# Performance work log

Hardware: AMD Instinct MI355X
Metric: run time of the kernel (lower is better)

## Reference

```python
import jax, jax.numpy as jnp
import numpy as np

D = 1024
S = 2048
B = 4


def setup_inputs() -> dict:
    key = jax.random.key(0)
    ks = jax.random.split(key, 9)
    sc = 1.0 / np.sqrt(D)
    return {
        "x": jax.random.normal(ks[0], (B, S, D), dtype=jnp.float32),
        "Wq": jax.random.normal(ks[1], (D, D), dtype=jnp.float32) * sc,
        "bq": jax.random.normal(ks[2], (D,), dtype=jnp.float32) * 0.02,
        "Wk": jax.random.normal(ks[3], (D, D), dtype=jnp.float32) * sc,
        "bk": jax.random.normal(ks[4], (D,), dtype=jnp.float32) * 0.02,
        "Wv": jax.random.normal(ks[5], (D, D), dtype=jnp.float32) * sc,
        "bv": jax.random.normal(ks[6], (D,), dtype=jnp.float32) * 0.02,
        "Wp": jax.random.normal(ks[7], (D, D), dtype=jnp.float32) * sc,
        "bp": jax.random.normal(ks[8], (D,), dtype=jnp.float32) * 0.02,
    }


def reference(x, Wq, bq, Wk, bk, Wv, bv, Wp, bp):
    # torch nn.Linear: y = x @ W.T + b  (W stored [out, in])
    q = jnp.einsum("bsd,ed->bse", x, Wq) + bq  # [B,S,D]
    k = jnp.einsum("bsd,ed->bse", x, Wk) + bk
    v = jnp.einsum("bsd,ed->bse", x, Wv) + bv

    scale = 1.0 / jnp.sqrt(jnp.asarray(q.shape[-1], q.dtype))
    # single-head attention: contract over full embd_dim (no head split in source)
    scores = jnp.einsum("bqd,bkd->bqk", q, k) * scale  # [B,S,S]

    seq = x.shape[1]
    causal = jnp.tril(jnp.ones((seq, seq), dtype=bool))  # [S,S]
    scores = jnp.where(causal[None, :, :], scores, -jnp.inf)

    attn = jax.nn.softmax(scores, axis=-1)  # [B,S,S]
    out = jnp.einsum("bqk,bkd->bqd", attn, v)  # [B,S,D]
    out = jnp.einsum("bsd,ed->bse", out, Wp) + bp
    return out
```

## Files before the change

### kernel.cpp

```cpp
#include <hip/hip_runtime.h>

#define AS1(p) ((const __attribute__((address_space(1))) void*)(p))
#define AS3(p) ((__attribute__((address_space(3))) void*)(p))

typedef unsigned short u16;
typedef __bf16 bf16x8 __attribute__((ext_vector_type(8)));
typedef short s16x8 __attribute__((ext_vector_type(8)));
typedef float f32x4 __attribute__((ext_vector_type(4)));
typedef unsigned short u16x4 __attribute__((ext_vector_type(4)));

__device__ __forceinline__ u16 f2bf(float x) {
    unsigned u = __float_as_uint(x);
    unsigned r = (u + 0x7FFFu + ((u >> 16) & 1u)) >> 16;
    return (u16)r;
}

template <typename V8>
__device__ __forceinline__ auto mfma_sel(V8 a, V8 b, f32x4 c, int)
    -> decltype(__builtin_amdgcn_mfma_f32_16x16x32_bf16(a, b, c, 0, 0, 0))
{
    return __builtin_amdgcn_mfma_f32_16x16x32_bf16(a, b, c, 0, 0, 0);
}
template <typename V8>
__device__ __forceinline__ f32x4 mfma_sel(V8 a, V8 b, f32x4 c, long)
{
    s16x8 a2 = __builtin_bit_cast(s16x8, a);
    s16x8 b2 = __builtin_bit_cast(s16x8, b);
    return __builtin_amdgcn_mfma_f32_16x16x32_bf16(a2, b2, c, 0, 0, 0);
}
__device__ __forceinline__ f32x4 mfma16x16x32(bf16x8 a, bf16x8 b, f32x4 c)
{
    return mfma_sel(a, b, c, 0);
}

__global__ __launch_bounds__(256) void cvt_bf16_kernel(const float* __restrict__ in,
                                                       u16* __restrict__ out, int n4)
{
    int i = blockIdx.x * 256 + threadIdx.x;
    if (i >= n4) return;
    float4 f = ((const float4*)in)[i];
    u16x4 o;
    o.x = f2bf(f.x); o.y = f2bf(f.y); o.z = f2bf(f.z); o.w = f2bf(f.w);
    ((u16x4*)out)[i] = o;
}

__global__ __launch_bounds__(256) void cvt_w4_kernel(const float* __restrict__ Wq,
                                                     const float* __restrict__ Wk,
                                                     const float* __restrict__ Wv,
                                                     const float* __restrict__ Wp,
                                                     u16* __restrict__ Wcat,
                                                     u16* __restrict__ Wpb, int n4)
{
    int i = blockIdx.x * 256 + threadIdx.x;
    if (i >= n4) return;
    const int by = blockIdx.y;
    const float* src = (by == 0) ? Wq : (by == 1) ? Wk : (by == 2) ? Wv : Wp;
    u16* dst = (by == 3) ? Wpb : (Wcat + (size_t)by * n4 * 4);
    float4 f = ((const float4*)src)[i];
    u16x4 o;
    o.x = f2bf(f.x); o.y = f2bf(f.y); o.z = f2bf(f.z); o.w = f2bf(f.w);
    ((u16x4*)dst)[i] = o;
}

#define GBM 128
#define GBN 256
#define GBK 64
#define ABUF 16384
#define BBUF 32768
#define TBUF (ABUF + BBUF)
#define LDS_NT2 (3 * TBUF)

template <int BIAS, int OUTBF16, int CSKIP, int CKB>
__global__ __launch_bounds__(512, 2)
void gemm_nt2(const u16* __restrict__ A, const u16* __restrict__ B,
              void* __restrict__ Cv, const float* __restrict__ bias,
              void* __restrict__ C2, const float* __restrict__ bias2,
              void* __restrict__ C3, const float* __restrict__ bias3,
              int M, int N, int K, int lda, int ldb, int ldc,
              long long sA, long long sB, long long sC, float scale)
{
    extern __shared__ char smem[];

    int by = blockIdx.y;
    if (CKB) by = gridDim.y - 1 - by;
    const int m0 = by * GBM;
    const int n0 = blockIdx.x * GBN;
    if (CSKIP && n0 > m0 + GBM - 1) return;

    const int z = blockIdx.z;
    A += (size_t)z * (size_t)sA;
    B += (size_t)z * (size_t)sB;

    const int t = threadIdx.x;
    const int lane = t & 63;
    const int w = t >> 6;
    const int wr = w >> 2;
    const int wc = w & 3;
    const int fr = lane & 15, fg = lane >> 4;

    int Keff = K;
    if (CKB) { Keff = m0 + GBM; if (Keff > K) Keff = K; }
    const int nk = Keff / GBK;

    f32x4 acc[4][4] = {};

    auto STAGE = [&](int kt, int buf) {
        const int k0 = kt * GBK;
        char* sb = smem + buf * TBUF;
        #pragma unroll
        for (int i = 0; i < 2; ++i) {
            int c = t + i * 512;
            int row = c >> 3;
            int sl = (c & 7) ^ (row & 7);
            __builtin_amdgcn_global_load_lds(
                AS1(A + (size_t)(m0 + row) * lda + k0 + sl * 8),
                AS3(sb + c * 16), 16, 0, 0);
        }
        #pragma unroll
        for (int i = 0; i < 4; ++i) {
            int c = t + i * 512;
            int row = c >> 3;
            int sl = (c & 7) ^ (row & 7);
            __builtin_amdgcn_global_load_lds(
                AS1(B + (size_t)(n0 + row) * ldb + k0 + sl * 8),
                AS3(sb + ABUF + c * 16), 16, 0, 0);
        }
    };

    STAGE(0, 0);
    STAGE(1, 1);
    asm volatile("s_waitcnt vmcnt(6)" ::: "memory");
    __builtin_amdgcn_s_barrier();

    int cur = 0;
    for (int kt = 0; kt < nk; ++kt) {
        int pb = cur + 2; if (pb >= 3) pb -= 3;
        const bool pf = (kt + 2 < nk);
        if (pf) STAGE(kt + 2, pb);

        const char* la = smem + cur * TBUF;
        const char* lb = la + ABUF;
        #pragma unroll
        for (int kk = 0; kk < GBK; kk += 32) {
            const int cs = (kk >> 3) + fg;
            bf16x8 af[4], bfv[4];
            #pragma unroll
            for (int mi = 0; mi < 4; ++mi) {
                int row = wr * 64 + mi * 16 + fr;
                af[mi] = *(const bf16x8*)(la + (row << 7) + ((cs ^ (row & 7)) << 4));
            }
            #pragma unroll
            for (int ni = 0; ni < 4; ++ni) {
                int row = wc * 64 + ni * 16 + fr;
                bfv[ni] = *(const bf16x8*)(lb + (row << 7) + ((cs ^ (row & 7)) << 4));
            }
            __builtin_amdgcn_s_setprio(1);
            #pragma unroll
            for (int mi = 0; mi < 4; ++mi)
                #pragma unroll
                for (int ni = 0; ni < 4; ++ni)
                    acc[mi][ni] = mfma16x16x32(af[mi], bfv[ni], acc[mi][ni]);
            __builtin_amdgcn_s_setprio(0);
        }

        if (pf) asm volatile("s_waitcnt vmcnt(6)" ::: "memory");
        else    asm volatile("s_waitcnt vmcnt(0)" ::: "memory");
        __builtin_amdgcn_s_barrier();
        ++cur; if (cur >= 3) cur = 0;
    }

    #pragma unroll
    for (int mi = 0; mi < 4; ++mi) {
        #pragma unroll
        for (int ni = 0; ni < 4; ++ni) {
            int col = n0 + wc * 64 + ni * 16 + fr;
            int row0 = m0 + wr * 64 + mi * 16 + fg * 4;
            if (BIAS == 3) {
                int seg = col >> 10;
                int ccol = col & 1023;
                if (seg == 0) {
                    float b = bias[ccol];
                    #pragma unroll
                    for (int j = 0; j < 4; ++j)
                        ((u16*)Cv)[(size_t)(row0 + j) * 1024 + ccol] =
                            f2bf((acc[mi][ni][j] + b) * scale);
                } else if (seg == 1) {
                    float b = bias2[ccol];
                    #pragma unroll
                    for (int j = 0; j < 4; ++j)
                        ((u16*)C2)[(size_t)(row0 + j) * 1024 + ccol] =
                            f2bf(acc[mi][ni][j] + b);
                } else {
                    float b = bias3[ccol];
                    u16x4 o;
                    #pragma unroll
                    for (int j = 0; j < 4; ++j) o[j] = f2bf(acc[mi][ni][j] + b);
                    *(u16x4*)&((u16*)C3)[(size_t)ccol * M + row0] = o;
                }
            } else {
                float bval = (BIAS == 1) ? bias[col] : 0.f;
                #pragma unroll
                for (int j = 0; j < 4; ++j) {
                    float v = (acc[mi][ni][j] + bval) * scale;
                    size_t off = (size_t)z * (size_t)sC + (size_t)(row0 + j) * ldc + col;
                    if (OUTBF16) ((u16*)Cv)[off] = f2bf(v);
                    else         ((float*)Cv)[off] = v;
                }
            }
        }
    }
}

__device__ __forceinline__ float waveMax(float v) {
    #pragma unroll
    for (int o = 32; o > 0; o >>= 1) v = fmaxf(v, __shfl_xor(v, o));
    return v;
}
__device__ __forceinline__ float waveSum(float v) {
    #pragma unroll
    for (int o = 32; o > 0; o >>= 1) v += __shfl_xor(v, o);
    return v;
}

__global__ __launch_bounds__(256) void softmax_causal_kernel(float* __restrict__ scores, int S)
{
    __shared__ float red[4];
    const int gb = blockIdx.x;
    const int b = gb / S;
    const int i = gb - b * S;
    float* srow = scores + (size_t)b * S * S + (size_t)i * S;
    u16* prow = (u16*)srow;
    const int t = threadIdx.x;
    const int jlim = ((i >> 7) + 1) << 7;

    float vals[8];
    float mx = -1e30f;
    #pragma unroll
    for (int s = 0; s < 8; ++s) {
        int j = t + (s << 8);
        float x = -1e30f;
        if (j <= i) x = srow[j];
        vals[s] = x;
        mx = fmaxf(mx, x);
    }
    mx = waveMax(mx);
    const int wv = t >> 6;
    if ((t & 63) == 0) red[wv] = mx;
    __syncthreads();
    mx = fmaxf(fmaxf(red[0], red[1]), fmaxf(red[2], red[3]));
    __syncthreads();

    float sum = 0.f;
    #pragma unroll
    for (int s = 0; s < 8; ++s) {
        float e = (vals[s] > -1e29f) ? __expf(vals[s] - mx) : 0.f;
        vals[s] = e;
        sum += e;
    }
    sum = waveSum(sum);
    if ((t & 63) == 0) red[wv] = sum;
    __syncthreads();
    sum = red[0] + red[1] + red[2] + red[3];
    const float inv = 1.f / sum;
    __syncthreads();

    #pragma unroll
    for (int s = 0; s < 8; ++s) {
        int j = t + (s << 8);
        if (j < jlim) prow[j] = f2bf(vals[s] * inv);
    }
}

extern "C" void kernel_launch(void* const* d_in, const int* in_sizes, int n_in,
                              void* d_out, int out_size, void* d_ws, size_t ws_size,
                              hipStream_t stream)
{
    (void)in_sizes; (void)n_in; (void)out_size;
    const float* x  = (const float*)d_in[0];
    const float* Wq = (const float*)d_in[1];
    const float* bq = (const float*)d_in[2];
    const float* Wk = (const float*)d_in[3];
    const float* bk = (const float*)d_in[4];
    const float* Wv = (const float*)d_in[5];
    const float* bv = (const float*)d_in[6];
    const float* Wp = (const float*)d_in[7];
    const float* bp = (const float*)d_in[8];

    const int D = 1024, S = 2048, B = 4;
    const int M = B * S;

    char* p = (char*)d_ws;
    u16* xb   = (u16*)p; p += (size_t)M * D * 2;
    u16* Wcat = (u16*)p; p += (size_t)3 * D * D * 2;
    u16* Wpb  = (u16*)p; p += (size_t)D * D * 2;
    u16* qb   = (u16*)p; p += (size_t)M * D * 2;
    u16* kb   = (u16*)p; p += (size_t)M * D * 2;
    u16* vTb  = (u16*)p; p += (size_t)M * D * 2;
    float* sc = (float*)p;
    u16* attnb = xb;

    const size_t fixed = (size_t)p - (size_t)d_ws;
    const size_t sb1   = (size_t)S * S * 4;
    int zb = (ws_size >= fixed + 4 * sb1) ? 4
           : (ws_size >= fixed + 2 * sb1) ? 2 : 1;

    hipFuncSetAttribute((const void*)gemm_nt2<3, 1, 0, 0>,
                        hipFuncAttributeMaxDynamicSharedMemorySize, LDS_NT2);
    hipFuncSetAttribute((const void*)gemm_nt2<0, 0, 1, 0>,
                        hipFuncAttributeMaxDynamicSharedMemorySize, LDS_NT2);
    hipFuncSetAttribute((const void*)gemm_nt2<0, 1, 0, 1>,
                        hipFuncAttributeMaxDynamicSharedMemorySize, LDS_NT2);
    hipFuncSetAttribute((const void*)gemm_nt2<1, 0, 0, 0>,
                        hipFuncAttributeMaxDynamicSharedMemorySize, LDS_NT2);

    cvt_bf16_kernel<<<(M * D / 4 + 255) / 256, 256, 0, stream>>>(x, xb, M * D / 4);
    cvt_w4_kernel<<<dim3((D * D / 4 + 255) / 256, 4), 256, 0, stream>>>(
        Wq, Wk, Wv, Wp, Wcat, Wpb, D * D / 4);

    gemm_nt2<3, 1, 0, 0><<<dim3(3 * D / GBN, M / GBM, 1), 512, LDS_NT2, stream>>>(
        xb, Wcat, qb, bq, kb, bk, vTb, bv,
        M, 3 * D, D, D, D, D, 0, 0, 0, 0.03125f);

    for (int b0 = 0; b0 < B; b0 += zb) {
        gemm_nt2<0, 0, 1, 0><<<dim3(S / GBN, S / GBM, zb), 512, LDS_NT2, stream>>>(
            qb + (size_t)b0 * S * D, kb + (size_t)b0 * S * D, sc, nullptr,
            nullptr, nullptr, nullptr, nullptr,
            S, S, D, D, D, S,
            (long long)S * D, (long long)S * D, (long long)S * S, 1.0f);
        softmax_causal_kernel<<<zb * S, 256, 0, stream>>>(sc, S);
        gemm_nt2<0, 1, 0, 1><<<dim3(D / GBN, S / GBM, zb), 512, LDS_NT2, stream>>>(
            (const u16*)sc, vTb + (size_t)b0 * S, attnb + (size_t)b0 * S * D, nullptr,
            nullptr, nullptr, nullptr, nullptr,
            S, D, S, 2 * S, M, D,
            (long long)2 * S * S, (long long)S, (long long)S * D, 1.0f);
    }

    gemm_nt2<1, 0, 0, 0><<<dim3(D / GBN, M / GBM, 1), 512, LDS_NT2, stream>>>(
        attnb, Wpb, d_out, bp, nullptr, nullptr, nullptr, nullptr,
        M, D, D, D, D, D, 0, 0, 0, 1.0f);
}
```

Measured before the change: 202.3 us.

## Store attention scores in bf16 and transpose V in a separate kernel

The QK^T GEMM now writes bf16 scores instead of fp32, which halves the traffic on the score matrix for both the softmax and the PV GEMM. The softmax is rewritten to read and write eight contiguous bf16 values per thread and to skip fully masked chunks. V is written row-major by the QKV GEMM and then transposed by a new LDS-tiled kernel, replacing the scattered transposed stores in the GEMM epilogue. This adds a kernel launch and an extra pass over V, and rounding the pre-softmax scores to bf16 costs some accuracy.

```diff
diff --git a/kernel.cpp b/kernel.cpp
--- a/kernel.cpp
+++ b/kernel.cpp
@@ -8,11 +8,15 @@
 typedef short s16x8 __attribute__((ext_vector_type(8)));
 typedef float f32x4 __attribute__((ext_vector_type(4)));
 typedef unsigned short u16x4 __attribute__((ext_vector_type(4)));
+typedef unsigned short u16x8v __attribute__((ext_vector_type(8)));
 
 __device__ __forceinline__ u16 f2bf(float x) {
     unsigned u = __float_as_uint(x);
     unsigned r = (u + 0x7FFFu + ((u >> 16) & 1u)) >> 16;
     return (u16)r;
+}
+__device__ __forceinline__ float bf2f(u16 x) {
+    return __uint_as_float(((unsigned)x) << 16);
 }
 
 template <typename V8>
@@ -60,6 +64,29 @@
     u16x4 o;
     o.x = f2bf(f.x); o.y = f2bf(f.y); o.z = f2bf(f.z); o.w = f2bf(f.w);
     ((u16x4*)dst)[i] = o;
+}
+
+__global__ __launch_bounds__(256) void transpose16(const u16* __restrict__ in,
+                                                   u16* __restrict__ out, int R, int C)
+{
+    __shared__ u16 tl[64][65];
+    const int tr0 = blockIdx.y * 64, tc0 = blockIdx.x * 64;
+    const int t = threadIdx.x;
+    const int r = t >> 2, c4 = (t & 3) << 4;
+
+    const u16* src = in + (size_t)(tr0 + r) * C + tc0 + c4;
+    u16x8v a0 = *(const u16x8v*)src;
+    u16x8v a1 = *(const u16x8v*)(src + 8);
+    #pragma unroll
+    for (int j = 0; j < 8; ++j) { tl[r][c4 + j] = a0[j]; tl[r][c4 + 8 + j] = a1[j]; }
+    __syncthreads();
+
+    u16x8v b0, b1;
+    #pragma unroll
+    for (int j = 0; j < 8; ++j) { b0[j] = tl[c4 + j][r]; b1[j] = tl[c4 + 8 + j][r]; }
+    u16* dst = out + (size_t)(tc0 + r) * R + tr0 + c4;
+    *(u16x8v*)dst = b0;
+    *(u16x8v*)(dst + 8) = b1;
 }
 
 #define GBM 128
@@ -178,25 +205,13 @@
             if (BIAS == 3) {
                 int seg = col >> 10;
                 int ccol = col & 1023;
-                if (seg == 0) {
-                    float b = bias[ccol];
-                    #pragma unroll
-                    for (int j = 0; j < 4; ++j)
-                        ((u16*)Cv)[(size_t)(row0 + j) * 1024 + ccol] =
-                            f2bf((acc[mi][ni][j] + b) * scale);
-                } else if (seg == 1) {
-                    float b = bias2[ccol];
-                    #pragma unroll
-                    for (int j = 0; j < 4; ++j)
-                        ((u16*)C2)[(size_t)(row0 + j) * 1024 + ccol] =
-                            f2bf(acc[mi][ni][j] + b);
-                } else {
-                    float b = bias3[ccol];
-                    u16x4 o;
-                    #pragma unroll
-                    for (int j = 0; j < 4; ++j) o[j] = f2bf(acc[mi][ni][j] + b);
-                    *(u16x4*)&((u16*)C3)[(size_t)ccol * M + row0] = o;
-                }
+                u16* dst = (seg == 0) ? (u16*)Cv : (seg == 1) ? (u16*)C2 : (u16*)C3;
+                float b = ((seg == 0) ? bias : (seg == 1) ? bias2 : bias3)[ccol];
+                float sc_ = (seg == 0) ? scale : 1.f;
+                #pragma unroll
+                for (int j = 0; j < 4; ++j)
+                    dst[(size_t)(row0 + j) * 1024 + ccol] =
+                        f2bf((acc[mi][ni][j] + b) * sc_);
             } else {
                 float bval = (BIAS == 1) ? bias[col] : 0.f;
                 #pragma unroll
@@ -222,27 +237,33 @@
     return v;
 }
 
-__global__ __launch_bounds__(256) void softmax_causal_kernel(float* __restrict__ scores, int S)
+__global__ __launch_bounds__(256) void softmax_causal_bf16(u16* __restrict__ scores, int S)
 {
     __shared__ float red[4];
     const int gb = blockIdx.x;
     const int b = gb / S;
     const int i = gb - b * S;
-    float* srow = scores + (size_t)b * S * S + (size_t)i * S;
-    u16* prow = (u16*)srow;
+    u16* row = scores + (size_t)b * S * S + (size_t)i * S;
     const int t = threadIdx.x;
     const int jlim = ((i >> 7) + 1) << 7;
-
-    float vals[8];
+    const int j0 = t << 3;
+    const bool act = j0 < jlim;
+
+    float v[8];
     float mx = -1e30f;
-    #pragma unroll
-    for (int s = 0; s < 8; ++s) {
-        int j = t + (s << 8);
-        float x = -1e30f;
-        if (j <= i) x = srow[j];
-        vals[s] = x;
-        mx = fmaxf(mx, x);
-    }
+    if (act) {
+        u16x8v raw = *(const u16x8v*)(row + j0);
+        #pragma unroll
+        for (int e = 0; e < 8; ++e) {
+            float x = bf2f(raw[e]);
+            v[e] = (j0 + e <= i) ? x : -1e30f;
+            mx = fmaxf(mx, v[e]);
+        }
+    } else {
+        #pragma unroll
+        for (int e = 0; e < 8; ++e) v[e] = -1e30f;
+    }
+
     mx = waveMax(mx);
     const int wv = t >> 6;
     if ((t & 63) == 0) red[wv] = mx;
@@ -251,23 +272,25 @@
     __syncthreads();
 
     float sum = 0.f;
-    #pragma unroll
-    for (int s = 0; s < 8; ++s) {
-        float e = (vals[s] > -1e29f) ? __expf(vals[s] - mx) : 0.f;
-        vals[s] = e;
-        sum += e;
+    if (act) {
+        #pragma unroll
+        for (int e = 0; e < 8; ++e) {
+            float ex = (v[e] > -1e29f) ? __expf(v[e] - mx) : 0.f;
+            v[e] = ex;
+            sum += ex;
+        }
     }
     sum = waveSum(sum);
     if ((t & 63) == 0) red[wv] = sum;
     __syncthreads();
     sum = red[0] + red[1] + red[2] + red[3];
     const float inv = 1.f / sum;
-    __syncthreads();
-
-    #pragma unroll
-    for (int s = 0; s < 8; ++s) {
-        int j = t + (s << 8);
-        if (j < jlim) prow[j] = f2bf(vals[s] * inv);
+
+    if (act) {
+        u16x8v o;
+        #pragma unroll
+        for (int e = 0; e < 8; ++e) o[e] = f2bf(v[e] * inv);
+        *(u16x8v*)(row + j0) = o;
     }
 }
 
@@ -296,17 +319,19 @@
     u16* qb   = (u16*)p; p += (size_t)M * D * 2;
     u16* kb   = (u16*)p; p += (size_t)M * D * 2;
     u16* vTb  = (u16*)p; p += (size_t)M * D * 2;
-    float* sc = (float*)p;
+    u16* vb   = (u16*)p;
+    u16* sc   = (u16*)p;
     u16* attnb = xb;
 
     const size_t fixed = (size_t)p - (size_t)d_ws;
-    const size_t sb1   = (size_t)S * S * 4;
-    int zb = (ws_size >= fixed + 4 * sb1) ? 4
-           : (ws_size >= fixed + 2 * sb1) ? 2 : 1;
+    const size_t sb1   = (size_t)S * S * 2;
+    const size_t vbsz  = (size_t)M * D * 2;
+    int zb = (ws_size >= fixed + (4 * sb1 > vbsz ? 4 * sb1 : vbsz)) ? 4
+           : (ws_size >= fixed + (2 * sb1 > vbsz ? 2 * sb1 : vbsz)) ? 2 : 1;
 
     hipFuncSetAttribute((const void*)gemm_nt2<3, 1, 0, 0>,
                         hipFuncAttributeMaxDynamicSharedMemorySize, LDS_NT2);
-    hipFuncSetAttribute((const void*)gemm_nt2<0, 0, 1, 0>,
+    hipFuncSetAttribute((const void*)gemm_nt2<0, 1, 1, 0>,
                         hipFuncAttributeMaxDynamicSharedMemorySize, LDS_NT2);
     hipFuncSetAttribute((const void*)gemm_nt2<0, 1, 0, 1>,
                         hipFuncAttributeMaxDynamicSharedMemorySize, LDS_NT2);
@@ -318,21 +343,23 @@
         Wq, Wk, Wv, Wp, Wcat, Wpb, D * D / 4);
 
     gemm_nt2<3, 1, 0, 0><<<dim3(3 * D / GBN, M / GBM, 1), 512, LDS_NT2, stream>>>(
-        xb, Wcat, qb, bq, kb, bk, vTb, bv,
+        xb, Wcat, qb, bq, kb, bk, vb, bv,
         M, 3 * D, D, D, D, D, 0, 0, 0, 0.03125f);
 
+    transpose16<<<dim3(D / 64, M / 64), 256, 0, stream>>>(vb, vTb, M, D);
+
     for (int b0 = 0; b0 < B; b0 += zb) {
-        gemm_nt2<0, 0, 1, 0><<<dim3(S / GBN, S / GBM, zb), 512, LDS_NT2, stream>>>(
+        gemm_nt2<0, 1, 1, 0><<<dim3(S / GBN, S / GBM, zb), 512, LDS_NT2, stream>>>(
             qb + (size_t)b0 * S * D, kb + (size_t)b0 * S * D, sc, nullptr,
             nullptr, nullptr, nullptr, nullptr,
             S, S, D, D, D, S,
             (long long)S * D, (long long)S * D, (long long)S * S, 1.0f);
-        softmax_causal_kernel<<<zb * S, 256, 0, stream>>>(sc, S);
+        softmax_causal_bf16<<<zb * S, 256, 0, stream>>>(sc, S);
         gemm_nt2<0, 1, 0, 1><<<dim3(D / GBN, S / GBM, zb), 512, LDS_NT2, stream>>>(
-            (const u16*)sc, vTb + (size_t)b0 * S, attnb + (size_t)b0 * S * D, nullptr,
+            sc, vTb + (size_t)b0 * S, attnb + (size_t)b0 * S * D, nullptr,
             nullptr, nullptr, nullptr, nullptr,
-            S, D, S, 2 * S, M, D,
-            (long long)2 * S * S, (long long)S, (long long)S * D, 1.0f);
+            S, D, S, S, M, D,
+            (long long)S * S, (long long)S, (long long)S * D, 1.0f);
     }
 
     gemm_nt2<1, 0, 0, 0><<<dim3(D / GBN, M / GBM, 1), 512, LDS_NT2, stream>>>(
```

After: 200.7 us. About the same (-0.8%).
